# Kernel optimization log

Measured on AMD Instinct MI355X. Metric: run time of the kernel, lower is better.

## Reference

```python
import jax, jax.numpy as jnp
import numpy as np
from math import sqrt

T_TEMP = 1.0  # softmax temperature (init arg T)
NEG_INF = -1e30  # finite stand-in for -inf; masked probs are exactly 0 after softmax


def setup_inputs() -> dict:
    key = jax.random.key(0)
    kq, kk, kv = jax.random.split(key, 3)
    B, L, H, E = 4, 2048, 16, 64
    queries = jax.random.normal(kq, (B, L, H, E), dtype=jnp.float32)
    keys = jax.random.normal(kk, (B, L, H, E), dtype=jnp.float32)
    values = jax.random.normal(kv, (B, L, H, E), dtype=jnp.float32)
    return {"queries": queries, "keys": keys, "values": values}


def reference(queries, keys, values):
    # queries: [B,L,H,E], keys: [B,S,H,E], values: [B,S,H,D]
    B, L, H, E = queries.shape
    S = keys.shape[1]
    scale = 1.0 / sqrt(E)
    # scores: [B,H,L,S]
    scores = jnp.einsum('blhe,bshe->bhls', queries, keys) * scale
    # causal mask: True above diagonal -> masked out (TriangularCausalMask)
    causal = jnp.triu(jnp.ones((L, S), dtype=bool), k=1)
    scores = jnp.where(causal, NEG_INF, scores)
    A = jax.nn.softmax(scores / T_TEMP, axis=-1)  # dropout p=0 -> identity
    V = jnp.einsum('bhls,bshd->blhd', A, values)
    return V
```

## Files before the change

### kernel.cpp

```cpp
#include <hip/hip_runtime.h>


typedef __attribute__((ext_vector_type(8))) unsigned short u16x8;
typedef __attribute__((ext_vector_type(4))) unsigned short u16x4;
typedef __attribute__((ext_vector_type(8))) __bf16 bf16x8;
typedef __attribute__((ext_vector_type(4))) float f32x4;
typedef __attribute__((ext_vector_type(16))) float f32x16;
typedef __attribute__((ext_vector_type(4))) unsigned int u32x4;

#define LOG2E 1.44269504088896340736f
#define AS1 __attribute__((address_space(1)))
#define AS3 __attribute__((address_space(3)))

static __device__ __forceinline__ unsigned short f32_bf16_rne(float x) {
    unsigned int b = __builtin_bit_cast(unsigned int, x);
    b = (b + 0x7fffu + ((b >> 16) & 1u)) >> 16;
    return (unsigned short)b;
}

static __device__ __forceinline__ unsigned int cvt_pk_bf16(float lo, float hi) {
    unsigned int r;
    asm("v_cvt_pk_bf16_f32 %0, %1, %2" : "=v"(r) : "v"(lo), "v"(hi));
    return r;
}

static __device__ __forceinline__ int swzs(int row) {
    return (row & 6) | ((row >> 3) & 1);
}
static __device__ __forceinline__ int tileIdx(int row, int col) {
    return row * 64 + (((col >> 3) ^ swzs(row)) << 3) + (col & 7);
}

__global__ __launch_bounds__(256) void prep_kernel(
    const float* __restrict__ K, const float* __restrict__ V,
    unsigned short* __restrict__ wsK, unsigned short* __restrict__ wsV)
{
    const int ROW = 1024;
    const int tid = threadIdx.x;
    const int kt  = blockIdx.x;
    const int bh  = blockIdx.y;
    const size_t tileBase = (size_t)(bh >> 4) * 2048 * ROW + (size_t)(bh & 15) * 64
                          + (size_t)(kt * 64) * ROW;
    unsigned short* kimg = wsK + (((size_t)bh * 32 + kt) << 12);
    unsigned short* vimg = wsV + (((size_t)bh * 32 + kt) << 12);

    __shared__ __align__(16) unsigned short ik[4096];
    __shared__ unsigned int sT[64 * 33];

    {
        const int key = tid & 63, ec = tid >> 6;
        const float* kr = K + tileBase + (size_t)key * ROW + ec * 16;
        #pragma unroll
        for (int i = 0; i < 4; ++i) {
            f32x4 v = *(const f32x4*)(kr + 4 * i);
            u16x4 w;
            #pragma unroll
            for (int j = 0; j < 4; ++j) w[j] = f32_bf16_rne(v[j]);
            const int e = ec * 16 + 4 * i;
            *(u16x4*)&ik[(e >> 3) * 512 + key * 8 + (e & 7)] = w;
        }
    }

    {
        const int kp = tid & 31, d0 = (tid >> 5) * 8;
        const float* v0 = V + tileBase + (size_t)(2 * kp) * ROW + d0;
        f32x4 a0 = *(const f32x4*)(v0);
        f32x4 a1 = *(const f32x4*)(v0 + 4);
        f32x4 b0 = *(const f32x4*)(v0 + ROW);
        f32x4 b1 = *(const f32x4*)(v0 + ROW + 4);
        #pragma unroll
        for (int i = 0; i < 4; ++i) {
            sT[(d0 + i) * 33 + kp]     = cvt_pk_bf16(a0[i], b0[i]);
            sT[(d0 + 4 + i) * 33 + kp] = cvt_pk_bf16(a1[i], b1[i]);
        }
    }
    __syncthreads();

    {
        const u32x4* src = (const u32x4*)ik;
        u32x4* dst = (u32x4*)kimg;
        dst[tid]       = src[tid];
        dst[256 + tid] = src[256 + tid];
    }
    {
        u32x4* vd = (u32x4*)vimg;
        u32x4 w0, w1;
        #pragma unroll
        for (int j = 0; j < 4; ++j) {
            const int unit = tid;
            const int kc8 = unit >> 6, dx = unit & 63;
            const int d = dx ^ kc8, kp = kc8 * 4 + j;
            w0[j] = sT[d * 33 + kp];
        }
        #pragma unroll
        for (int j = 0; j < 4; ++j) {
            const int unit = 256 + tid;
            const int kc8 = unit >> 6, dx = unit & 63;
            const int d = dx ^ kc8, kp = kc8 * 4 + j;
            w1[j] = sT[d * 33 + kp];
        }
        vd[tid]       = w0;
        vd[256 + tid] = w1;
    }
}

__global__ __launch_bounds__(128, 4) void fattn2_kernel(
    const float* __restrict__ Q,
    const unsigned short* __restrict__ wsK,
    const unsigned short* __restrict__ wsV,
    float* __restrict__ O)
{
    const int ROW = 1024;

    const int tid  = threadIdx.x;
    const int wave = tid >> 6;
    const int lane = tid & 63;
    const int s    = lane >> 5;
    const int n32  = lane & 31;
    const bool hi32 = (s != 0);

    const int id    = blockIdx.x;
    const int qtile = 31 - (id >> 6);
    const int bh    = id & 63;
    const size_t headBase = (size_t)(bh >> 4) * 2048 * ROW + (size_t)(bh & 15) * 64;
    const int q0 = qtile * 64 + wave * 32;

    __shared__ __align__(16) unsigned short sK[2][4096];
    __shared__ __align__(16) unsigned short sV[2][4096];

    const int kbase = s * 1024 + n32 * 16;
    int vbase[4];
    #pragma unroll
    for (int c = 0; c < 4; ++c)
        vbase[c] = c * 2048 + s * 1024 + ((n32 ^ (2 * c + s)) << 4);

    const float c0 = 0.125f * LOG2E;

    bf16x8 qf[4];
    {
        const float* qrow = Q + headBase + (size_t)(q0 + n32) * ROW + s * 8;
        #pragma unroll
        for (int c = 0; c < 4; ++c) {
            f32x4 v0 = *(const f32x4*)(qrow + 16 * c);
            f32x4 v1 = *(const f32x4*)(qrow + 16 * c + 4);
            u32x4 a;
            a[0] = cvt_pk_bf16(v0[0] * c0, v0[1] * c0);
            a[1] = cvt_pk_bf16(v0[2] * c0, v0[3] * c0);
            a[2] = cvt_pk_bf16(v1[0] * c0, v1[1] * c0);
            a[3] = cvt_pk_bf16(v1[2] * c0, v1[3] * c0);
            qf[c] = __builtin_bit_cast(bf16x8, a);
        }
    }

    f32x16 oacc0, oacc1;
    #pragma unroll
    for (int r = 0; r < 16; ++r) { oacc0[r] = 0.f; oacc1[r] = 0.f; }
    float l = 0.f;

    const int nT = qtile + 1;

    #define STAGE(buf, kt_)                                                    \
    do {                                                                       \
        const size_t toff = (((size_t)bh * 32 + (kt_)) << 12);                 \
        const unsigned short* kg = wsK + toff + wave * 2048 + lane * 8;        \
        const unsigned short* vg = wsV + toff + wave * 2048 + lane * 8;        \
        __builtin_amdgcn_global_load_lds((const AS1 unsigned int*)kg,          \
            (AS3 unsigned int*)&sK[buf][wave * 2048], 16, 0, 0);               \
        __builtin_amdgcn_global_load_lds((const AS1 unsigned int*)(kg + 512),  \
            (AS3 unsigned int*)&sK[buf][wave * 2048 + 512], 16, 0, 0);         \
        __builtin_amdgcn_global_load_lds((const AS1 unsigned int*)(kg + 1024), \
            (AS3 unsigned int*)&sK[buf][wave * 2048 + 1024], 16, 0, 0);        \
        __builtin_amdgcn_global_load_lds((const AS1 unsigned int*)(kg + 1536), \
            (AS3 unsigned int*)&sK[buf][wave * 2048 + 1536], 16, 0, 0);        \
        __builtin_amdgcn_global_load_lds((const AS1 unsigned int*)vg,          \
            (AS3 unsigned int*)&sV[buf][wave * 2048], 16, 0, 0);               \
        __builtin_amdgcn_global_load_lds((const AS1 unsigned int*)(vg + 512),  \
            (AS3 unsigned int*)&sV[buf][wave * 2048 + 512], 16, 0, 0);         \
        __builtin_amdgcn_global_load_lds((const AS1 unsigned int*)(vg + 1024), \
            (AS3 unsigned int*)&sV[buf][wave * 2048 + 1024], 16, 0, 0);        \
        __builtin_amdgcn_global_load_lds((const AS1 unsigned int*)(vg + 1536), \
            (AS3 unsigned int*)&sV[buf][wave * 2048 + 1536], 16, 0, 0);        \
    } while (0)

    STAGE(0, 0);

    for (int kt = 0; kt < nT; ++kt) {
        const int cur = kt & 1;

        __syncthreads();

        if (kt + 1 < nT) STAGE(cur ^ 1, kt + 1);

        const char* kb = (const char*)&sK[cur][0];
        const char* vb = (const char*)&sV[cur][0];

        f32x16 s0v, s1v;
        #pragma unroll
        for (int r = 0; r < 16; ++r) { s0v[r] = 0.f; s1v[r] = 0.f; }
        #pragma unroll
        for (int c = 0; c < 4; ++c) {
            bf16x8 k0 = __builtin_bit_cast(bf16x8,
                *(const u16x8*)(kb + kbase + c * 2048));
            bf16x8 k1 = __builtin_bit_cast(bf16x8,
                *(const u16x8*)(kb + kbase + c * 2048 + 512));
            s0v = __builtin_amdgcn_mfma_f32_32x32x16_bf16(k0, qf[c], s0v, 0, 0, 0);
            s1v = __builtin_amdgcn_mfma_f32_32x32x16_bf16(k1, qf[c], s1v, 0, 0, 0);
        }

        if (kt == qtile) {
            const int ql = wave * 32 + n32;
            #pragma unroll
            for (int r = 0; r < 16; ++r) {
                const int k0 = (r & 3) + 8 * (r >> 2) + 4 * s;
                s0v[r] = (k0 > ql) ? -1e30f : s0v[r];
                s1v[r] = (k0 + 32 > ql) ? -1e30f : s1v[r];
            }
        }

        float la = 0.f, lb = 0.f;
        #pragma unroll
        for (int r = 0; r < 16; ++r) {
            s0v[r] = __builtin_amdgcn_exp2f(s0v[r]);
            s1v[r] = __builtin_amdgcn_exp2f(s1v[r]);
            la += s0v[r];
            lb += s1v[r];
        }
        l += la + lb;

        bf16x8 bp[4];
        #define XCHG(pe, cc, DST)                                              \
        do {                                                                   \
            unsigned int P0 = cvt_pk_bf16(pe[8*(cc)+0], pe[8*(cc)+1]);         \
            unsigned int P1 = cvt_pk_bf16(pe[8*(cc)+2], pe[8*(cc)+3]);         \
            unsigned int P2 = cvt_pk_bf16(pe[8*(cc)+4], pe[8*(cc)+5]);         \
            unsigned int P3 = cvt_pk_bf16(pe[8*(cc)+6], pe[8*(cc)+7]);         \
            unsigned int x0 = __shfl_xor(P0, 32, 64);                          \
            unsigned int x1 = __shfl_xor(P1, 32, 64);                          \
            unsigned int x2 = __shfl_xor(P2, 32, 64);                          \
            unsigned int x3 = __shfl_xor(P3, 32, 64);                          \
            u32x4 bw;                                                          \
            bw[0] = hi32 ? x2 : P0;                                            \
            bw[1] = hi32 ? x3 : P1;                                            \
            bw[2] = hi32 ? P2 : x0;                                            \
            bw[3] = hi32 ? P3 : x1;                                            \
            DST = __builtin_bit_cast(bf16x8, bw);                              \
        } while (0)
        XCHG(s0v, 0, bp[0]);
        XCHG(s0v, 1, bp[1]);
        XCHG(s1v, 0, bp[2]);
        XCHG(s1v, 1, bp[3]);
        #undef XCHG

        #pragma unroll
        for (int c = 0; c < 4; ++c) {
            bf16x8 v0 = __builtin_bit_cast(bf16x8,
                *(const u16x8*)(vb + vbase[c]));
            bf16x8 v1 = __builtin_bit_cast(bf16x8,
                *(const u16x8*)(vb + vbase[c] + 512));
            oacc0 = __builtin_amdgcn_mfma_f32_32x32x16_bf16(v0, bp[c], oacc0, 0, 0, 0);
            oacc1 = __builtin_amdgcn_mfma_f32_32x32x16_bf16(v1, bp[c], oacc1, 0, 0, 0);
        }
    }
    #undef STAGE

    l += __shfl_xor(l, 32, 64);
    const float inv = 1.0f / l;

    __syncthreads();
    float* tb = wave ? (float*)&sV[0][0] : (float*)&sK[0][0];
    #pragma unroll
    for (int r = 0; r < 16; ++r) {
        const int d0 = (r & 3) + 8 * (r >> 2) + 4 * s;
        tb[n32 * 68 + d0]      = oacc0[r] * inv;
        tb[n32 * 68 + d0 + 32] = oacc1[r] * inv;
    }
    #pragma unroll
    for (int it = 0; it < 8; ++it) {
        const int row = (lane >> 2) + 16 * (it & 1);
        const int c4  = (lane & 3) + 4 * (it >> 1);
        f32x4 v = *(const f32x4*)&tb[row * 68 + c4 * 4];
        *(f32x4*)&O[headBase + (size_t)(q0 + row) * ROW + c4 * 4] = v;
    }
}

__global__ __launch_bounds__(256, 4) void fattn_kernel(
    const float* __restrict__ Q,
    const float* __restrict__ K,
    const float* __restrict__ V,
    float* __restrict__ O)
{
    const int ROW = 1024;
    const int tid  = threadIdx.x;
    const int wave = tid >> 6;
    const int lane = tid & 63;
    const int quad = lane >> 4;
    const int n16  = lane & 15;
    const int xb = blockIdx.x;
    const int bh = blockIdx.y;
    const size_t headBase = (size_t)(bh >> 4) * 2048 * ROW + (size_t)(bh & 15) * 64;

    __shared__ __align__(16) unsigned short sK[4096];
    __shared__ __align__(16) unsigned short sV[4096];
    __shared__ __align__(16) unsigned short sP[4][1024];

    int kvIdx[4];
    #pragma unroll
    for (int nb = 0; nb < 4; ++nb) {
        const int row = nb * 16 + n16;
        kvIdx[nb] = row * 64 + ((quad ^ swzs(row)) << 3);
    }
    const int pIdx = n16 * 64 + ((quad ^ swzs(n16)) << 3);
    const int kStageRow = tid >> 4;
    const int kStageCol = (tid & 15) * 4;
    const int vKey2  = (tid & 31) * 2;
    const int vDbase = (tid >> 5) * 8;
    const float c0 = 0.125f * LOG2E;

    for (int qi = 0; qi < 2; ++qi) {
        const int qtile = qi ? (31 - xb) : xb;
        const int q0 = qtile * 64 + wave * 16;
        bf16x8 qf0, qf1;
        {
            const float* qrow = Q + headBase + (size_t)(q0 + n16) * ROW + quad * 8;
            u16x8 a, b;
            #pragma unroll
            for (int i = 0; i < 8; ++i) {
                a[i] = f32_bf16_rne(qrow[i] * c0);
                b[i] = f32_bf16_rne(qrow[32 + i] * c0);
            }
            qf0 = __builtin_bit_cast(bf16x8, a);
            qf1 = __builtin_bit_cast(bf16x8, b);
        }
        f32x4 oacc[4];
        #pragma unroll
        for (int d = 0; d < 4; ++d) oacc[d] = (f32x4){0.f, 0.f, 0.f, 0.f};
        float l_r[4];
        #pragma unroll
        for (int r = 0; r < 4; ++r) l_r[r] = 0.f;
        const int nT = qtile + 1;
        f32x4 pk[4], pva[2], pvb[2];
        {
            const float* kb = K + headBase;
            const float* r0 = V + headBase + (size_t)vKey2 * ROW + vDbase;
            #pragma unroll
            for (int j = 0; j < 4; ++j)
                pk[j] = *(const f32x4*)(kb + (size_t)(j * 16 + kStageRow) * ROW + kStageCol);
            #pragma unroll
            for (int j = 0; j < 2; ++j) {
                pva[j] = *(const f32x4*)(r0 + j * 4);
                pvb[j] = *(const f32x4*)(r0 + ROW + j * 4);
            }
        }
        for (int kt = 0; kt < nT; ++kt) {
            __syncthreads();
            #pragma unroll
            for (int j = 0; j < 4; ++j) {
                u16x4 w;
                #pragma unroll
                for (int i = 0; i < 4; ++i) w[i] = f32_bf16_rne(pk[j][i]);
                *(u16x4*)&sK[tileIdx(j * 16 + kStageRow, kStageCol)] = w;
            }
            #pragma unroll
            for (int j = 0; j < 2; ++j) {
                const int d0 = vDbase + j * 4;
                #pragma unroll
                for (int i = 0; i < 4; ++i) {
                    unsigned int pkk = (unsigned int)f32_bf16_rne(pva[j][i])
                                     | ((unsigned int)f32_bf16_rne(pvb[j][i]) << 16);
                    *(unsigned int*)&sV[tileIdx(d0 + i, vKey2)] = pkk;
                }
            }
            if (kt + 1 < nT) {
                const size_t nb2 = headBase + (size_t)((kt + 1) * 64) * ROW;
                const float* kb = K + nb2;
                const float* r0 = V + nb2 + (size_t)vKey2 * ROW + vDbase;
                #pragma unroll
                for (int j = 0; j < 4; ++j)
                    pk[j] = *(const f32x4*)(kb + (size_t)(j * 16 + kStageRow) * ROW + kStageCol);
                #pragma unroll
                for (int j = 0; j < 2; ++j) {
                    pva[j] = *(const f32x4*)(r0 + j * 4);
                    pvb[j] = *(const f32x4*)(r0 + ROW + j * 4);
                }
            }
            __syncthreads();
            f32x4 sacc[4];
            #pragma unroll
            for (int nb = 0; nb < 4; ++nb) {
                bf16x8 b0 = __builtin_bit_cast(bf16x8, *(const u16x8*)&sK[kvIdx[nb]]);
                bf16x8 b1 = __builtin_bit_cast(bf16x8, *(const u16x8*)&sK[kvIdx[nb] ^ 32]);
                f32x4 ss = (f32x4){0.f, 0.f, 0.f, 0.f};
                ss = __builtin_amdgcn_mfma_f32_16x16x32_bf16(qf0, b0, ss, 0, 0, 0);
                ss = __builtin_amdgcn_mfma_f32_16x16x32_bf16(qf1, b1, ss, 0, 0, 0);
                sacc[nb] = ss;
            }
            if (kt == qtile) {
                #pragma unroll
                for (int nb = 0; nb < 4; ++nb) {
                    const int keyl = nb * 16 + n16;
                    #pragma unroll
                    for (int r = 0; r < 4; ++r) {
                        const int ql = wave * 16 + quad * 4 + r;
                        sacc[nb][r] = (keyl > ql) ? -1e30f : sacc[nb][r];
                    }
                }
            }
            #pragma unroll
            for (int r = 0; r < 4; ++r) {
                const int qrl = quad * 4 + r;
                const int pwBase = qrl * 64 + (n16 & 7);
                const int sw = swzs(qrl);
                const int hb = n16 >> 3;
                float ps = 0.f;
                #pragma unroll
                for (int nb = 0; nb < 4; ++nb) {
                    unsigned short u = f32_bf16_rne(__builtin_amdgcn_exp2f(sacc[nb][r]));
                    ps += __builtin_bit_cast(float, (unsigned int)u << 16);
                    sP[wave][pwBase + (((nb * 2 + hb) ^ sw) << 3)] = u;
                }
                l_r[r] += ps;
            }
            #pragma unroll
            for (int kh = 0; kh < 2; ++kh) {
                bf16x8 ap = __builtin_bit_cast(bf16x8,
                    *(const u16x8*)&sP[wave][pIdx ^ (kh << 5)]);
                #pragma unroll
                for (int d = 0; d < 4; ++d) {
                    bf16x8 vf = __builtin_bit_cast(bf16x8,
                        *(const u16x8*)&sV[kvIdx[d] ^ (kh << 5)]);
                    oacc[d] = __builtin_amdgcn_mfma_f32_16x16x32_bf16(ap, vf, oacc[d], 0, 0, 0);
                }
            }
        }
        float inv[4];
        #pragma unroll
        for (int r = 0; r < 4; ++r) {
            float l = l_r[r];
            #pragma unroll
            for (int off = 1; off < 16; off <<= 1)
                l += __shfl_xor(l, off, 64);
            inv[r] = 1.0f / l;
        }
        #pragma unroll
        for (int d = 0; d < 4; ++d) {
            #pragma unroll
            for (int r = 0; r < 4; ++r) {
                const int qg = q0 + quad * 4 + r;
                O[headBase + (size_t)qg * ROW + d * 16 + n16] = oacc[d][r] * inv[r];
            }
        }
    }
}

extern "C" void kernel_launch(void* const* d_in, const int* in_sizes, int n_in,
                              void* d_out, int out_size, void* d_ws, size_t ws_size,
                              hipStream_t stream) {
    const float* Q = (const float*)d_in[0];
    const float* K = (const float*)d_in[1];
    const float* V = (const float*)d_in[2];
    float* Out = (float*)d_out;

    const size_t imgElems = (size_t)64 * 32 * 4096;
    if (ws_size >= imgElems * 2 * sizeof(unsigned short)) {
        unsigned short* wsK = (unsigned short*)d_ws;
        unsigned short* wsV = wsK + imgElems;
        hipLaunchKernelGGL(prep_kernel, dim3(32, 64), dim3(256), 0, stream, K, V, wsK, wsV);
        hipLaunchKernelGGL(fattn2_kernel, dim3(2048), dim3(128), 0, stream, Q, wsK, wsV, Out);
    } else {
        hipLaunchKernelGGL(fattn_kernel, dim3(16, 64), dim3(256), 0, stream, Q, K, V, Out);
    }
}
```

Baseline: 197.8 us.

## Split key tile across four waves with cross-wave output reduction

Doubles the block to four waves: each pair of waves shares a 32-row query slice, and each wave handles half of the 64-key tile. The halves are combined at the end through a swizzled LDS reduction of the partial outputs and row sums. The diagonal tile's fully masked half is skipped, and s_setprio is raised around the MFMA sections. This aims to increase parallelism and latency hiding per block, at the cost of an extra LDS reduction and synchronisation, and adds a clamp on exponent inputs.

```diff
diff --git a/kernel.cpp b/kernel.cpp
--- a/kernel.cpp
+++ b/kernel.cpp
@@ -104,7 +104,7 @@
     }
 }
 
-__global__ __launch_bounds__(128, 4) void fattn2_kernel(
+__global__ __launch_bounds__(256, 4) void fattn2_kernel(
     const float* __restrict__ Q,
     const unsigned short* __restrict__ wsK,
     const unsigned short* __restrict__ wsV,
@@ -118,21 +118,24 @@
     const int s    = lane >> 5;
     const int n32  = lane & 31;
     const bool hi32 = (s != 0);
+    const int qh = wave & 1;
+    const int kh = wave >> 1;
 
     const int id    = blockIdx.x;
     const int qtile = 31 - (id >> 6);
     const int bh    = id & 63;
     const size_t headBase = (size_t)(bh >> 4) * 2048 * ROW + (size_t)(bh & 15) * 64;
-    const int q0 = qtile * 64 + wave * 32;
+    const int q0 = qtile * 64 + qh * 32;
 
     __shared__ __align__(16) unsigned short sK[2][4096];
     __shared__ __align__(16) unsigned short sV[2][4096];
 
-    const int kbase = s * 1024 + n32 * 16;
-    int vbase[4];
+    const int kBase = s * 1024 + n32 * 16 + kh * 512;
+    int vbB[2];
     #pragma unroll
-    for (int c = 0; c < 4; ++c)
-        vbase[c] = c * 2048 + s * 1024 + ((n32 ^ (2 * c + s)) << 4);
+    for (int c = 0; c < 2; ++c)
+        vbB[c] = kh * 4096 + c * 2048 + s * 1024
+               + ((n32 ^ (4 * kh + 2 * c + s)) << 4);
 
     const float c0 = 0.125f * LOG2E;
 
@@ -162,24 +165,16 @@
     #define STAGE(buf, kt_)                                                    \
     do {                                                                       \
         const size_t toff = (((size_t)bh * 32 + (kt_)) << 12);                 \
-        const unsigned short* kg = wsK + toff + wave * 2048 + lane * 8;        \
-        const unsigned short* vg = wsV + toff + wave * 2048 + lane * 8;        \
+        const unsigned short* kg = wsK + toff + wave * 1024 + lane * 8;        \
+        const unsigned short* vg = wsV + toff + wave * 1024 + lane * 8;        \
         __builtin_amdgcn_global_load_lds((const AS1 unsigned int*)kg,          \
-            (AS3 unsigned int*)&sK[buf][wave * 2048], 16, 0, 0);               \
+            (AS3 unsigned int*)&sK[buf][wave * 1024], 16, 0, 0);               \
         __builtin_amdgcn_global_load_lds((const AS1 unsigned int*)(kg + 512),  \
-            (AS3 unsigned int*)&sK[buf][wave * 2048 + 512], 16, 0, 0);         \
-        __builtin_amdgcn_global_load_lds((const AS1 unsigned int*)(kg + 1024), \
-            (AS3 unsigned int*)&sK[buf][wave * 2048 + 1024], 16, 0, 0);        \
-        __builtin_amdgcn_global_load_lds((const AS1 unsigned int*)(kg + 1536), \
-            (AS3 unsigned int*)&sK[buf][wave * 2048 + 1536], 16, 0, 0);        \
+            (AS3 unsigned int*)&sK[buf][wave * 1024 + 512], 16, 0, 0);         \
         __builtin_amdgcn_global_load_lds((const AS1 unsigned int*)vg,          \
-            (AS3 unsigned int*)&sV[buf][wave * 2048], 16, 0, 0);               \
+            (AS3 unsigned int*)&sV[buf][wave * 1024], 16, 0, 0);               \
         __builtin_amdgcn_global_load_lds((const AS1 unsigned int*)(vg + 512),  \
-            (AS3 unsigned int*)&sV[buf][wave * 2048 + 512], 16, 0, 0);         \
-        __builtin_amdgcn_global_load_lds((const AS1 unsigned int*)(vg + 1024), \
-            (AS3 unsigned int*)&sV[buf][wave * 2048 + 1024], 16, 0, 0);        \
-        __builtin_amdgcn_global_load_lds((const AS1 unsigned int*)(vg + 1536), \
-            (AS3 unsigned int*)&sV[buf][wave * 2048 + 1536], 16, 0, 0);        \
+            (AS3 unsigned int*)&sV[buf][wave * 1024 + 512], 16, 0, 0);         \
     } while (0)
 
     STAGE(0, 0);
@@ -191,43 +186,40 @@
 
         if (kt + 1 < nT) STAGE(cur ^ 1, kt + 1);
 
+        if (kt == qtile && kh > qh) continue;
+
         const char* kb = (const char*)&sK[cur][0];
         const char* vb = (const char*)&sV[cur][0];
 
-        f32x16 s0v, s1v;
-        #pragma unroll
-        for (int r = 0; r < 16; ++r) { s0v[r] = 0.f; s1v[r] = 0.f; }
+        f32x16 sacc;
+        #pragma unroll
+        for (int r = 0; r < 16; ++r) sacc[r] = 0.f;
+        __builtin_amdgcn_s_setprio(1);
         #pragma unroll
         for (int c = 0; c < 4; ++c) {
             bf16x8 k0 = __builtin_bit_cast(bf16x8,
-                *(const u16x8*)(kb + kbase + c * 2048));
-            bf16x8 k1 = __builtin_bit_cast(bf16x8,
-                *(const u16x8*)(kb + kbase + c * 2048 + 512));
-            s0v = __builtin_amdgcn_mfma_f32_32x32x16_bf16(k0, qf[c], s0v, 0, 0, 0);
-            s1v = __builtin_amdgcn_mfma_f32_32x32x16_bf16(k1, qf[c], s1v, 0, 0, 0);
-        }
-
-        if (kt == qtile) {
-            const int ql = wave * 32 + n32;
+                *(const u16x8*)(kb + kBase + c * 2048));
+            sacc = __builtin_amdgcn_mfma_f32_32x32x16_bf16(k0, qf[c], sacc, 0, 0, 0);
+        }
+        __builtin_amdgcn_s_setprio(0);
+
+        if (kt == qtile && kh == qh) {
             #pragma unroll
             for (int r = 0; r < 16; ++r) {
                 const int k0 = (r & 3) + 8 * (r >> 2) + 4 * s;
-                s0v[r] = (k0 > ql) ? -1e30f : s0v[r];
-                s1v[r] = (k0 + 32 > ql) ? -1e30f : s1v[r];
-            }
-        }
-
-        float la = 0.f, lb = 0.f;
+                sacc[r] = (k0 > n32) ? -1e30f : sacc[r];
+            }
+        }
+
+        float la = 0.f;
         #pragma unroll
         for (int r = 0; r < 16; ++r) {
-            s0v[r] = __builtin_amdgcn_exp2f(s0v[r]);
-            s1v[r] = __builtin_amdgcn_exp2f(s1v[r]);
-            la += s0v[r];
-            lb += s1v[r];
-        }
-        l += la + lb;
-
-        bf16x8 bp[4];
+            sacc[r] = __builtin_amdgcn_exp2f(fminf(sacc[r], 80.f));
+            la += sacc[r];
+        }
+        l += la;
+
+        bf16x8 bp[2];
         #define XCHG(pe, cc, DST)                                              \
         do {                                                                   \
             unsigned int P0 = cvt_pk_bf16(pe[8*(cc)+0], pe[8*(cc)+1]);         \
@@ -245,41 +237,72 @@
             bw[3] = hi32 ? P3 : x1;                                            \
             DST = __builtin_bit_cast(bf16x8, bw);                              \
         } while (0)
-        XCHG(s0v, 0, bp[0]);
-        XCHG(s0v, 1, bp[1]);
-        XCHG(s1v, 0, bp[2]);
-        XCHG(s1v, 1, bp[3]);
+        XCHG(sacc, 0, bp[0]);
+        XCHG(sacc, 1, bp[1]);
         #undef XCHG
 
-        #pragma unroll
-        for (int c = 0; c < 4; ++c) {
+        __builtin_amdgcn_s_setprio(1);
+        #pragma unroll
+        for (int c = 0; c < 2; ++c) {
             bf16x8 v0 = __builtin_bit_cast(bf16x8,
-                *(const u16x8*)(vb + vbase[c]));
+                *(const u16x8*)(vb + vbB[c]));
             bf16x8 v1 = __builtin_bit_cast(bf16x8,
-                *(const u16x8*)(vb + vbase[c] + 512));
+                *(const u16x8*)(vb + vbB[c] + 512));
             oacc0 = __builtin_amdgcn_mfma_f32_32x32x16_bf16(v0, bp[c], oacc0, 0, 0, 0);
             oacc1 = __builtin_amdgcn_mfma_f32_32x32x16_bf16(v1, bp[c], oacc1, 0, 0, 0);
         }
+        __builtin_amdgcn_s_setprio(0);
     }
     #undef STAGE
 
     l += __shfl_xor(l, 32, 64);
-    const float inv = 1.0f / l;
 
     __syncthreads();
-    float* tb = wave ? (float*)&sV[0][0] : (float*)&sK[0][0];
-    #pragma unroll
-    for (int r = 0; r < 16; ++r) {
-        const int d0 = (r & 3) + 8 * (r >> 2) + 4 * s;
-        tb[n32 * 68 + d0]      = oacc0[r] * inv;
-        tb[n32 * 68 + d0 + 32] = oacc1[r] * inv;
-    }
-    #pragma unroll
-    for (int it = 0; it < 8; ++it) {
-        const int row = (lane >> 2) + 16 * (it & 1);
-        const int c4  = (lane & 3) + 4 * (it >> 1);
-        f32x4 v = *(const f32x4*)&tb[row * 68 + c4 * 4];
-        *(f32x4*)&O[headBase + (size_t)(q0 + row) * ROW + c4 * 4] = v;
+
+    float* lbuf = (float*)&sV[0][0];
+    lbuf[wave * 32 + n32] = l;
+    float* tb = (float*)&sK[0][0] + qh * 2048;
+    if (kh == 1) {
+        #pragma unroll
+        for (int rr = 0; rr < 4; ++rr) {
+            f32x4 w0, w1;
+            #pragma unroll
+            for (int j = 0; j < 4; ++j) {
+                w0[j] = oacc0[4 * rr + j];
+                w1[j] = oacc1[4 * rr + j];
+            }
+            const int s40 = 2 * rr + s;
+            const int s41 = 8 + 2 * rr + s;
+            *(f32x4*)&tb[n32 * 64 + ((s40 ^ (n32 & 15)) << 2)] = w0;
+            *(f32x4*)&tb[n32 * 64 + ((s41 ^ (n32 & 15)) << 2)] = w1;
+        }
+    }
+    __syncthreads();
+    if (kh == 0) {
+        const float inv = 1.0f / (l + lbuf[64 + qh * 32 + n32]);
+        #pragma unroll
+        for (int rr = 0; rr < 4; ++rr) {
+            const int s40 = 2 * rr + s;
+            const int s41 = 8 + 2 * rr + s;
+            float* a0 = &tb[n32 * 64 + ((s40 ^ (n32 & 15)) << 2)];
+            float* a1 = &tb[n32 * 64 + ((s41 ^ (n32 & 15)) << 2)];
+            f32x4 p0 = *(const f32x4*)a0;
+            f32x4 p1 = *(const f32x4*)a1;
+            #pragma unroll
+            for (int j = 0; j < 4; ++j) {
+                p0[j] = (p0[j] + oacc0[4 * rr + j]) * inv;
+                p1[j] = (p1[j] + oacc1[4 * rr + j]) * inv;
+            }
+            *(f32x4*)a0 = p0;
+            *(f32x4*)a1 = p1;
+        }
+        #pragma unroll
+        for (int it = 0; it < 8; ++it) {
+            const int row = (lane >> 2) + 16 * (it & 1);
+            const int c4  = (lane & 3) + 4 * (it >> 1);
+            f32x4 v = *(const f32x4*)&tb[row * 64 + ((c4 ^ (row & 15)) << 2)];
+            *(f32x4*)&O[headBase + (size_t)(q0 + row) * ROW + c4 * 4] = v;
+        }
     }
 }
 
@@ -465,7 +488,7 @@
         unsigned short* wsK = (unsigned short*)d_ws;
         unsigned short* wsV = wsK + imgElems;
         hipLaunchKernelGGL(prep_kernel, dim3(32, 64), dim3(256), 0, stream, K, V, wsK, wsV);
-        hipLaunchKernelGGL(fattn2_kernel, dim3(2048), dim3(128), 0, stream, Q, wsK, wsV, Out);
+        hipLaunchKernelGGL(fattn2_kernel, dim3(2048), dim3(256), 0, stream, Q, wsK, wsV, Out);
     } else {
         hipLaunchKernelGGL(fattn_kernel, dim3(16, 64), dim3(256), 0, stream, Q, K, V, Out);
     }
```

Result: faster. 191.3 us (-3.3%).
